# Kernel tuning notes

Hardware: AMD Instinct MI355X
Metric: run time of the kernel (lower is better)

## Reference

```python
import jax, jax.numpy as jnp
import numpy as np

N_HEADS = 8
N_HIDDEN = 32  # out_features // n_heads
NEG_SLOPE = 0.21
MASK_VAL = -1000000.0  # precision == '32'


def setup_inputs() -> dict:
    key = jax.random.key(0)
    k1, k2, k3, k4, k5 = jax.random.split(key, 5)
    B, N, Fin = 4, 512, 256
    HF = N_HEADS * N_HIDDEN
    h = jax.random.normal(k1, (B, N, Fin), dtype=jnp.float32)
    adj_mat = jax.random.randint(k2, (1, N, N, 1), 0, 2, dtype=jnp.int32)
    W_l = jax.random.normal(k3, (Fin, HF), dtype=jnp.float32) * 0.05
    W_r = jax.random.normal(k4, (Fin, HF), dtype=jnp.float32) * 0.05
    attn_w = jax.random.normal(k5, (N_HIDDEN,), dtype=jnp.float32) * 0.05
    return {"h": h, "adj_mat": adj_mat, "W_l": W_l, "W_r": W_r, "attn_w": attn_w}


def reference(h, adj_mat, W_l, W_r, attn_w):
    B, N, _ = h.shape
    H, F = N_HEADS, N_HIDDEN
    g_l = (h @ W_l).reshape(B, N, H, F)
    g_r = (h @ W_r).reshape(B, N, H, F)
    # torch repeat/repeat_interleave semantics: g_sum[b,i,j] = g_l[b,j] + g_r[b,i]
    g_sum = g_l[:, None, :, :, :] + g_r[:, :, None, :, :]  # (B, i, j, H, F)
    act = jnp.where(g_sum >= 0, g_sum, NEG_SLOPE * g_sum)
    e = jnp.einsum('bijhf,f->bijh', act, attn_w)  # (B, N, N, H)
    e = jnp.where(adj_mat == 0, MASK_VAL, e)
    a = jax.nn.softmax(e, axis=2)
    # dropout is identity in eval mode
    attn_res = jnp.einsum('bijh,bjhf->bihf', a, g_r)
    return attn_res.reshape(B, N, H * F)  # is_concat=True
```

## Files before the change

### kernel.cpp

```cpp
#include <hip/hip_runtime.h>
#include <math.h>

#define BB 4
#define NN 512
#define FIN 256
#define NH 8
#define FD 32
#define HF 256
#define MASKH (-60000.0f)
#define CA 0.605f
#define CB 0.395f
#define IT 32
#define ESTR 268
#define GTS 260

typedef _Float16 h2_t __attribute__((ext_vector_type(2)));
union H2U { unsigned u; h2_t h; };
typedef __fp16 v8h __attribute__((ext_vector_type(8)));
typedef float v4f __attribute__((ext_vector_type(4)));
union U8 { uint4 u4; v8h h; };

__device__ __forceinline__ h2_t pkrtz(float a, float b) {
  auto r = __builtin_amdgcn_cvt_pkrtz(a, b);
  union { decltype(r) f; h2_t h; } u;
  u.f = r;
  return u.h;
}
__device__ __forceinline__ unsigned pkrtz_u(float a, float b) {
  H2U u; u.h = pkrtz(a, b);
  return u.u;
}

__device__ __forceinline__ float acc2(unsigned g, h2_t q, h2_t u, float acc) {
  H2U v; v.u = g;
  h2_t s = v.h + q;
  H2U a; a.h = s; a.u &= 0x7fff7fffu;
  return __builtin_amdgcn_fdot2(a.h, u, acc, false);
}

__device__ __forceinline__ float score16(uint4 g0, uint4 g1, uint4 g2, uint4 g3,
                                         const h2_t* qh, const h2_t* uh,
                                         float init) {
  float e0 = init, e1 = 0.f;
  e0 = acc2(g0.x, qh[0], uh[0], e0);
  e1 = acc2(g0.y, qh[1], uh[1], e1);
  e0 = acc2(g0.z, qh[2], uh[2], e0);
  e1 = acc2(g0.w, qh[3], uh[3], e1);
  e0 = acc2(g1.x, qh[4], uh[4], e0);
  e1 = acc2(g1.y, qh[5], uh[5], e1);
  e0 = acc2(g1.z, qh[6], uh[6], e0);
  e1 = acc2(g1.w, qh[7], uh[7], e1);
  e0 = acc2(g2.x, qh[8], uh[8], e0);
  e1 = acc2(g2.y, qh[9], uh[9], e1);
  e0 = acc2(g2.z, qh[10], uh[10], e0);
  e1 = acc2(g2.w, qh[11], uh[11], e1);
  e0 = acc2(g3.x, qh[12], uh[12], e0);
  e1 = acc2(g3.y, qh[13], uh[13], e1);
  e0 = acc2(g3.z, qh[14], uh[14], e0);
  e1 = acc2(g3.w, qh[15], uh[15], e1);
  return e0 + e1;
}

__global__ __launch_bounds__(256) void gemm_dual(
    const float* __restrict__ h, const float* __restrict__ Wl,
    const float* __restrict__ Wr, _Float16* __restrict__ glh,
    _Float16* __restrict__ grh) {
  const int t = threadIdx.x;
  const int row0 = blockIdx.x * 8;
  const float* __restrict__ W = blockIdx.y ? Wr : Wl;

  float acc[8] = {0.f, 0.f, 0.f, 0.f, 0.f, 0.f, 0.f, 0.f};
  const float* Wp = W + t;
  const float* hp = h + (size_t)row0 * FIN;

#pragma unroll 2
  for (int k4 = 0; k4 < FIN / 4; ++k4) {
    float4 hv[8];
#pragma unroll
    for (int r = 0; r < 8; ++r)
      hv[r] = *(const float4*)(hp + r * FIN + 4 * k4);
#pragma unroll
    for (int kk = 0; kk < 4; ++kk) {
      const float w = Wp[(size_t)(4 * k4 + kk) * HF];
#pragma unroll
      for (int r = 0; r < 8; ++r) {
        const float hval = (kk == 0) ? hv[r].x
                         : (kk == 1) ? hv[r].y
                         : (kk == 2) ? hv[r].z : hv[r].w;
        acc[r] = fmaf(hval, w, acc[r]);
      }
    }
  }

  _Float16* gp = (blockIdx.y ? grh : glh) + (size_t)row0 * HF + t;
#pragma unroll
  for (int r = 0; r < 8; ++r) gp[(size_t)r * HF] = (_Float16)acc[r];
}

__global__ __launch_bounds__(256, 2) void gat_attn(
    const _Float16* __restrict__ glh, const _Float16* __restrict__ grh,
    const int* __restrict__ adj, const float* __restrict__ aw,
    float* __restrict__ out) {
  __shared__ __align__(16) unsigned ubuf[32 * GTS];
  __shared__ __align__(16) unsigned e_s[IT][ESTR];
  __shared__ float Al_s[NN];
  __shared__ float inv_l[IT];

  const int t = threadIdx.x;
  const int hh = blockIdx.x;
  const int i0 = blockIdx.y * IT;
  const int b = blockIdx.z;
  const int ii = t & 31;
  const int jg = t >> 5;

  uint4* gl4 = (uint4*)ubuf;

  const _Float16* glp = glh + (size_t)b * NN * HF + hh * FD;

  h2_t wv[16], uh[16], qh[16];
  float a_r = 0.f;
  {
#pragma unroll
    for (int f4 = 0; f4 < 8; ++f4) {
      const float4 w4 = *(const float4*)(aw + 4 * f4);
      wv[2 * f4] = pkrtz(CA * w4.x, CA * w4.y);
      wv[2 * f4 + 1] = pkrtz(CA * w4.z, CA * w4.w);
      uh[2 * f4] = pkrtz(CB * w4.x, CB * w4.y);
      uh[2 * f4 + 1] = pkrtz(CB * w4.z, CB * w4.w);
    }
    const uint4* qp4 =
        (const uint4*)(grh + (size_t)(b * NN + i0 + ii) * HF + hh * FD);
    const uint4 q0 = qp4[0], q1 = qp4[1], q2 = qp4[2], q3 = qp4[3];
    H2U z;
    z.u = q0.x; qh[0] = z.h;  z.u = q0.y; qh[1] = z.h;
    z.u = q0.z; qh[2] = z.h;  z.u = q0.w; qh[3] = z.h;
    z.u = q1.x; qh[4] = z.h;  z.u = q1.y; qh[5] = z.h;
    z.u = q1.z; qh[6] = z.h;  z.u = q1.w; qh[7] = z.h;
    z.u = q2.x; qh[8] = z.h;  z.u = q2.y; qh[9] = z.h;
    z.u = q2.z; qh[10] = z.h; z.u = q2.w; qh[11] = z.h;
    z.u = q3.x; qh[12] = z.h; z.u = q3.y; qh[13] = z.h;
    z.u = q3.z; qh[14] = z.h; z.u = q3.w; qh[15] = z.h;
#pragma unroll
    for (int f2 = 0; f2 < 16; ++f2)
      a_r = __builtin_amdgcn_fdot2(qh[f2], wv[f2], a_r, false);
  }

#pragma unroll
  for (int c = 0; c < 2; ++c) {
    const int j = t + 256 * c;
    const uint4* gp = (const uint4*)(glp + (size_t)j * HF);
    const uint4 g0 = gp[0], g1 = gp[1], g2 = gp[2], g3 = gp[3];
    gl4[0 * NN + j] = g0;
    gl4[1 * NN + j] = g1;
    gl4[2 * NN + j] = g2;
    gl4[3 * NN + j] = g3;
    float s0 = 0.f, s1 = 0.f;
    H2U v;
#define ALD(gu, i)                                                  \
  v.u = gu.x; s0 = __builtin_amdgcn_fdot2(v.h, wv[i+0], s0, false); \
  v.u = gu.y; s1 = __builtin_amdgcn_fdot2(v.h, wv[i+1], s1, false); \
  v.u = gu.z; s0 = __builtin_amdgcn_fdot2(v.h, wv[i+2], s0, false); \
  v.u = gu.w; s1 = __builtin_amdgcn_fdot2(v.h, wv[i+3], s1, false);
    ALD(g0, 0) ALD(g1, 4) ALD(g2, 8) ALD(g3, 12)
#undef ALD
    Al_s[j] = s0 + s1;
  }
  __syncthreads();

  {
    unsigned* erow = &e_s[ii][jg * 32];
    const int* adjp = adj + (size_t)(i0 + ii) * NN + jg * 64;
#pragma unroll 4
    for (int g4 = 0; g4 < 16; ++g4) {
      const int4 a4 = ((const int4*)adjp)[g4];
      const int j = jg * 64 + 4 * g4;
      float e0 = score16(gl4[0 * NN + j], gl4[1 * NN + j], gl4[2 * NN + j],
                         gl4[3 * NN + j], qh, uh, Al_s[j] + a_r);
      float e1 = score16(gl4[0 * NN + j + 1], gl4[1 * NN + j + 1],
                         gl4[2 * NN + j + 1], gl4[3 * NN + j + 1], qh, uh,
                         Al_s[j + 1] + a_r);
      float e2 = score16(gl4[0 * NN + j + 2], gl4[1 * NN + j + 2],
                         gl4[2 * NN + j + 2], gl4[3 * NN + j + 2], qh, uh,
                         Al_s[j + 2] + a_r);
      float e3 = score16(gl4[0 * NN + j + 3], gl4[1 * NN + j + 3],
                         gl4[2 * NN + j + 3], gl4[3 * NN + j + 3], qh, uh,
                         Al_s[j + 3] + a_r);
      e0 = a4.x ? e0 : MASKH;
      e1 = a4.y ? e1 : MASKH;
      e2 = a4.z ? e2 : MASKH;
      e3 = a4.w ? e3 : MASKH;
      erow[2 * g4] = pkrtz_u(e0, e1);
      erow[2 * g4 + 1] = pkrtz_u(e2, e3);
    }
  }
  __syncthreads();

  {
    const int fq = t & 7;
    const int jp0 = t >> 3;
    const unsigned* gbase =
        (const unsigned*)(grh + (size_t)b * NN * HF + hh * FD) + 2 * fq;
#pragma unroll
    for (int s2 = 0; s2 < 8; ++s2) {
      const int jp = jp0 + 32 * s2;
      const uint2 A = *(const uint2*)(gbase + (size_t)(2 * jp) * 128);
      const uint2 Bv = *(const uint2*)(gbase + (size_t)(2 * jp + 1) * 128);
      ubuf[(4 * fq + 0) * GTS + jp] = __builtin_amdgcn_perm(Bv.x, A.x, 0x05040100u);
      ubuf[(4 * fq + 1) * GTS + jp] = __builtin_amdgcn_perm(Bv.x, A.x, 0x07060302u);
      ubuf[(4 * fq + 2) * GTS + jp] = __builtin_amdgcn_perm(Bv.y, A.y, 0x05040100u);
      ubuf[(4 * fq + 3) * GTS + jp] = __builtin_amdgcn_perm(Bv.y, A.y, 0x07060302u);
    }
    const int row = t >> 3;
    const int l8 = t & 7;
    unsigned* erow = &e_s[row][0];
    float m = MASKH;
#pragma unroll
    for (int c = 0; c < 32; ++c) {
      H2U v; v.u = erow[l8 + 8 * c];
      m = fmaxf(m, fmaxf((float)v.h.x, (float)v.h.y));
    }
#pragma unroll
    for (int off = 1; off < 8; off <<= 1) m = fmaxf(m, __shfl_xor(m, off));
    float s = 0.f;
#pragma unroll
    for (int c = 0; c < 32; ++c) {
      H2U v; v.u = erow[l8 + 8 * c];
      const float p0 = __expf((float)v.h.x - m);
      const float p1 = __expf((float)v.h.y - m);
      s += p0 + p1;
      erow[l8 + 8 * c] = pkrtz_u(p0, p1);
    }
#pragma unroll
    for (int off = 1; off < 8; off <<= 1) s += __shfl_xor(s, off);
    if (l8 == 0) inv_l[row] = 1.f / s;
  }
  __syncthreads();

  {
    const int lane = t & 63;
    const int wv3 = t >> 6;
    const int Mt = wv3 & 1, Nt = wv3 >> 1;
    const int l16 = lane & 15, q = lane >> 4;
    const unsigned* arow = &e_s[Mt * 16 + l16][0];
    const unsigned* brow = &ubuf[(Nt * 16 + l16) * GTS];
    v4f acc = {0.f, 0.f, 0.f, 0.f};
#pragma unroll
    for (int s = 0; s < 16; ++s) {
      U8 a; a.u4 = *(const uint4*)(arow + 16 * s + 4 * q);
      U8 bf; bf.u4 = *(const uint4*)(brow + 16 * s + 4 * q);
      acc = __builtin_amdgcn_mfma_f32_16x16x32_f16(a.h, bf.h, acc, 0, 0, 0);
    }
    float* op = out + (size_t)(b * NN + i0 + Mt * 16 + q * 4) * HF + hh * FD +
                Nt * 16 + l16;
#pragma unroll
    for (int r = 0; r < 4; ++r) {
      op[(size_t)r * HF] = acc[r] * inv_l[Mt * 16 + q * 4 + r];
    }
  }
}

extern "C" void kernel_launch(void* const* d_in, const int* in_sizes, int n_in,
                              void* d_out, int out_size, void* d_ws,
                              size_t ws_size, hipStream_t stream) {
  const float* h = (const float*)d_in[0];
  const int* adj = (const int*)d_in[1];
  const float* Wl = (const float*)d_in[2];
  const float* Wr = (const float*)d_in[3];
  const float* aw = (const float*)d_in[4];
  float* out = (float*)d_out;

  _Float16* glh = (_Float16*)d_ws;
  _Float16* grh = (_Float16*)((char*)d_ws + (size_t)BB * NN * HF * 2);

  dim3 gg(BB * NN / 8, 2, 1);
  gemm_dual<<<gg, 256, 0, stream>>>(h, Wl, Wr, glh, grh);

  dim3 ga(NH, NN / IT, BB);
  gat_attn<<<ga, 256, 0, stream>>>(glh, grh, adj, aw, out);
}
```

Baseline: 105.1 us.

## Compute two query rows per thread, fuse exp into scoring, swizzle LDS

```diff
diff --git a/kernel.cpp b/kernel.cpp
--- a/kernel.cpp
+++ b/kernel.cpp
@@ -7,12 +7,13 @@
 #define NH 8
 #define FD 32
 #define HF 256
-#define MASKH (-60000.0f)
 #define CA 0.605f
 #define CB 0.395f
 #define IT 32
 #define ESTR 268
 #define GTS 260
+#define GLX(j) ((j) ^ (((j) >> 5) & 7))
+#define ALX(j) ((j) + ((j) >> 5))
 
 typedef _Float16 h2_t __attribute__((ext_vector_type(2)));
 union H2U { unsigned u; h2_t h; };
@@ -103,22 +104,23 @@
     float* __restrict__ out) {
   __shared__ __align__(16) unsigned ubuf[32 * GTS];
   __shared__ __align__(16) unsigned e_s[IT][ESTR];
-  __shared__ float Al_s[NN];
+  __shared__ float Al_s[544];
+  __shared__ float s_part[16][33];
   __shared__ float inv_l[IT];
 
   const int t = threadIdx.x;
   const int hh = blockIdx.x;
   const int i0 = blockIdx.y * IT;
   const int b = blockIdx.z;
-  const int ii = t & 31;
-  const int jg = t >> 5;
+  const int r0 = t & 15;
+  const int jg = t >> 4;
 
   uint4* gl4 = (uint4*)ubuf;
 
   const _Float16* glp = glh + (size_t)b * NN * HF + hh * FD;
 
-  h2_t wv[16], uh[16], qh[16];
-  float a_r = 0.f;
+  h2_t wv[16], uh[16], qh[16], qh2[16];
+  float a_r0 = 0.f, a_r1 = 0.f;
   {
 #pragma unroll
     for (int f4 = 0; f4 < 8; ++f4) {
@@ -128,9 +130,12 @@
       uh[2 * f4] = pkrtz(CB * w4.x, CB * w4.y);
       uh[2 * f4 + 1] = pkrtz(CB * w4.z, CB * w4.w);
     }
-    const uint4* qp4 =
-        (const uint4*)(grh + (size_t)(b * NN + i0 + ii) * HF + hh * FD);
-    const uint4 q0 = qp4[0], q1 = qp4[1], q2 = qp4[2], q3 = qp4[3];
+    const uint4* qa =
+        (const uint4*)(grh + (size_t)(b * NN + i0 + r0) * HF + hh * FD);
+    const uint4* qb =
+        (const uint4*)(grh + (size_t)(b * NN + i0 + r0 + 16) * HF + hh * FD);
+    const uint4 q0 = qa[0], q1 = qa[1], q2 = qa[2], q3 = qa[3];
+    const uint4 p0 = qb[0], p1 = qb[1], p2 = qb[2], p3 = qb[3];
     H2U z;
     z.u = q0.x; qh[0] = z.h;  z.u = q0.y; qh[1] = z.h;
     z.u = q0.z; qh[2] = z.h;  z.u = q0.w; qh[3] = z.h;
@@ -140,9 +145,19 @@
     z.u = q2.z; qh[10] = z.h; z.u = q2.w; qh[11] = z.h;
     z.u = q3.x; qh[12] = z.h; z.u = q3.y; qh[13] = z.h;
     z.u = q3.z; qh[14] = z.h; z.u = q3.w; qh[15] = z.h;
-#pragma unroll
-    for (int f2 = 0; f2 < 16; ++f2)
-      a_r = __builtin_amdgcn_fdot2(qh[f2], wv[f2], a_r, false);
+    z.u = p0.x; qh2[0] = z.h;  z.u = p0.y; qh2[1] = z.h;
+    z.u = p0.z; qh2[2] = z.h;  z.u = p0.w; qh2[3] = z.h;
+    z.u = p1.x; qh2[4] = z.h;  z.u = p1.y; qh2[5] = z.h;
+    z.u = p1.z; qh2[6] = z.h;  z.u = p1.w; qh2[7] = z.h;
+    z.u = p2.x; qh2[8] = z.h;  z.u = p2.y; qh2[9] = z.h;
+    z.u = p2.z; qh2[10] = z.h; z.u = p2.w; qh2[11] = z.h;
+    z.u = p3.x; qh2[12] = z.h; z.u = p3.y; qh2[13] = z.h;
+    z.u = p3.z; qh2[14] = z.h; z.u = p3.w; qh2[15] = z.h;
+#pragma unroll
+    for (int f2 = 0; f2 < 16; ++f2) {
+      a_r0 = __builtin_amdgcn_fdot2(qh[f2], wv[f2], a_r0, false);
+      a_r1 = __builtin_amdgcn_fdot2(qh2[f2], wv[f2], a_r1, false);
+    }
   }
 
 #pragma unroll
@@ -150,10 +165,11 @@
     const int j = t + 256 * c;
     const uint4* gp = (const uint4*)(glp + (size_t)j * HF);
     const uint4 g0 = gp[0], g1 = gp[1], g2 = gp[2], g3 = gp[3];
-    gl4[0 * NN + j] = g0;
-    gl4[1 * NN + j] = g1;
-    gl4[2 * NN + j] = g2;
-    gl4[3 * NN + j] = g3;
+    const int jx = GLX(j);
+    gl4[0 * NN + jx] = g0;
+    gl4[1 * NN + jx] = g1;
+    gl4[2 * NN + jx] = g2;
+    gl4[3 * NN + jx] = g3;
     float s0 = 0.f, s1 = 0.f;
     H2U v;
 #define ALD(gu, i)                                                  \
@@ -163,35 +179,47 @@
   v.u = gu.w; s1 = __builtin_amdgcn_fdot2(v.h, wv[i+3], s1, false);
     ALD(g0, 0) ALD(g1, 4) ALD(g2, 8) ALD(g3, 12)
 #undef ALD
-    Al_s[j] = s0 + s1;
+    Al_s[ALX(j)] = s0 + s1;
   }
   __syncthreads();
 
   {
-    unsigned* erow = &e_s[ii][jg * 32];
-    const int* adjp = adj + (size_t)(i0 + ii) * NN + jg * 64;
-#pragma unroll 4
-    for (int g4 = 0; g4 < 16; ++g4) {
-      const int4 a4 = ((const int4*)adjp)[g4];
-      const int j = jg * 64 + 4 * g4;
-      float e0 = score16(gl4[0 * NN + j], gl4[1 * NN + j], gl4[2 * NN + j],
-                         gl4[3 * NN + j], qh, uh, Al_s[j] + a_r);
-      float e1 = score16(gl4[0 * NN + j + 1], gl4[1 * NN + j + 1],
-                         gl4[2 * NN + j + 1], gl4[3 * NN + j + 1], qh, uh,
-                         Al_s[j + 1] + a_r);
-      float e2 = score16(gl4[0 * NN + j + 2], gl4[1 * NN + j + 2],
-                         gl4[2 * NN + j + 2], gl4[3 * NN + j + 2], qh, uh,
-                         Al_s[j + 2] + a_r);
-      float e3 = score16(gl4[0 * NN + j + 3], gl4[1 * NN + j + 3],
-                         gl4[2 * NN + j + 3], gl4[3 * NN + j + 3], qh, uh,
-                         Al_s[j + 3] + a_r);
-      e0 = a4.x ? e0 : MASKH;
-      e1 = a4.y ? e1 : MASKH;
-      e2 = a4.z ? e2 : MASKH;
-      e3 = a4.w ? e3 : MASKH;
-      erow[2 * g4] = pkrtz_u(e0, e1);
-      erow[2 * g4 + 1] = pkrtz_u(e2, e3);
-    }
+    unsigned* erow0 = &e_s[r0][jg * 16];
+    unsigned* erow1 = &e_s[r0 + 16][jg * 16];
+    const int* adjp0 = adj + (size_t)(i0 + r0) * NN + jg * 32;
+    const int* adjp1 = adj + (size_t)(i0 + r0 + 16) * NN + jg * 32;
+    float srow0 = 0.f, srow1 = 0.f;
+#pragma unroll 2
+    for (int g4 = 0; g4 < 8; ++g4) {
+      const int4 m0 = ((const int4*)adjp0)[g4];
+      const int4 m1 = ((const int4*)adjp1)[g4];
+      float p0[4], p1[4];
+#pragma unroll
+      for (int k = 0; k < 4; ++k) {
+        const int j = jg * 32 + 4 * g4 + k;
+        const int jx = GLX(j);
+        const uint4 g0 = gl4[0 * NN + jx], g1 = gl4[1 * NN + jx];
+        const uint4 g2 = gl4[2 * NN + jx], g3 = gl4[3 * NN + jx];
+        const float al = Al_s[ALX(j)];
+        const float e0 = score16(g0, g1, g2, g3, qh, uh, al + a_r0);
+        const float e1 = score16(g0, g1, g2, g3, qh2, uh, al + a_r1);
+        const int mk = (k == 0) ? m0.x : (k == 1) ? m0.y : (k == 2) ? m0.z : m0.w;
+        const int nk = (k == 0) ? m1.x : (k == 1) ? m1.y : (k == 2) ? m1.z : m1.w;
+        p0[k] = mk ? __expf(e0) : 0.f;
+        p1[k] = nk ? __expf(e1) : 0.f;
+      }
+      srow0 += (p0[0] + p0[1]) + (p0[2] + p0[3]);
+      srow1 += (p1[0] + p1[1]) + (p1[2] + p1[3]);
+      uint2 w0, w1;
+      w0.x = pkrtz_u(p0[0], p0[1]);
+      w0.y = pkrtz_u(p0[2], p0[3]);
+      w1.x = pkrtz_u(p1[0], p1[1]);
+      w1.y = pkrtz_u(p1[2], p1[3]);
+      *(uint2*)&erow0[2 * g4] = w0;
+      *(uint2*)&erow1[2 * g4] = w1;
+    }
+    s_part[jg][r0] = srow0;
+    s_part[jg][r0 + 16] = srow1;
   }
   __syncthreads();
 
@@ -210,29 +238,12 @@
       ubuf[(4 * fq + 2) * GTS + jp] = __builtin_amdgcn_perm(Bv.y, A.y, 0x05040100u);
       ubuf[(4 * fq + 3) * GTS + jp] = __builtin_amdgcn_perm(Bv.y, A.y, 0x07060302u);
     }
-    const int row = t >> 3;
-    const int l8 = t & 7;
-    unsigned* erow = &e_s[row][0];
-    float m = MASKH;
-#pragma unroll
-    for (int c = 0; c < 32; ++c) {
-      H2U v; v.u = erow[l8 + 8 * c];
-      m = fmaxf(m, fmaxf((float)v.h.x, (float)v.h.y));
-    }
-#pragma unroll
-    for (int off = 1; off < 8; off <<= 1) m = fmaxf(m, __shfl_xor(m, off));
-    float s = 0.f;
-#pragma unroll
-    for (int c = 0; c < 32; ++c) {
-      H2U v; v.u = erow[l8 + 8 * c];
-      const float p0 = __expf((float)v.h.x - m);
-      const float p1 = __expf((float)v.h.y - m);
-      s += p0 + p1;
-      erow[l8 + 8 * c] = pkrtz_u(p0, p1);
-    }
-#pragma unroll
-    for (int off = 1; off < 8; off <<= 1) s += __shfl_xor(s, off);
-    if (l8 == 0) inv_l[row] = 1.f / s;
+    if (t < IT) {
+      float s = 0.f;
+#pragma unroll
+      for (int c = 0; c < 16; ++c) s += s_part[c][t];
+      inv_l[t] = 1.f / s;
+    }
   }
   __syncthreads();
 
```

Result: no change. 104.0 us (median of 2 runs) (-1.1%).
